# Performance work log

Hardware: AMD Instinct MI355X
Metric: run time of the kernel (lower is better)

The kernel has to match this reference:

```python
import jax, jax.numpy as jnp
import numpy as np

NC = 30      # n_centres in HyperNetwork RBFs
WIDTH = 64
D = 32
BATCH = 1048576


def _rbf_linear(t, centres, log_sigmas, lin_w, lin_b):
    # RBF_CNF(in_features=1) followed by nn.Linear; gaussian basis exp(-d^2)
    d = jnp.abs(t - centres[:, 0]) / jnp.exp(log_sigmas)   # (NC,) via broadcast of t (1,)
    phi = jnp.exp(-d * d)
    return phi @ lin_w.T + lin_b                            # (out_features,)


def setup_inputs() -> dict:
    key = jax.random.key(0)
    blocksize = WIDTH * D
    ks = jax.random.split(key, 10)

    def lin(k, out_f, in_f):
        bound = 1.0 / np.sqrt(in_f).astype(np.float32)
        kw, kb = jax.random.split(k)
        w = jax.random.uniform(kw, (out_f, in_f), jnp.float32, -bound, bound)
        b = jax.random.uniform(kb, (out_f,), jnp.float32, -bound, bound)
        return w, b

    W_lin_w, W_lin_b = lin(ks[0], blocksize, NC)
    U_lin_w, U_lin_b = lin(ks[1], blocksize, NC)
    B_lin_w, B_lin_b = lin(ks[2], WIDTH, NC)
    return dict(
        t=jax.random.uniform(ks[3], (1,), jnp.float32),
        z=jax.random.normal(ks[4], (BATCH, D), jnp.float32),
        logp_z=jnp.zeros((BATCH, 1), jnp.float32),
        W_centres=jax.random.normal(ks[5], (NC, 1), jnp.float32),
        W_log_sigmas=jnp.zeros((NC,), jnp.float32),
        W_lin_w=W_lin_w, W_lin_b=W_lin_b,
        U_centres=jax.random.normal(ks[6], (NC, 1), jnp.float32),
        U_log_sigmas=jnp.zeros((NC,), jnp.float32),
        U_lin_w=U_lin_w, U_lin_b=U_lin_b,
        B_centres=jax.random.normal(ks[7], (NC, 1), jnp.float32),
        B_log_sigmas=jnp.zeros((NC,), jnp.float32),
        B_lin_w=B_lin_w, B_lin_b=B_lin_b,
    )


def reference(t, z, logp_z,
              W_centres, W_log_sigmas, W_lin_w, W_lin_b,
              U_centres, U_log_sigmas, U_lin_w, U_lin_b,
              B_centres, B_log_sigmas, B_lin_w, B_lin_b):
    # Hypernetwork-generated weights at time t
    Wt = _rbf_linear(t, W_centres, W_log_sigmas, W_lin_w, W_lin_b).reshape(WIDTH, D)
    Ut = _rbf_linear(t, U_centres, U_log_sigmas, U_lin_w, U_lin_b).reshape(WIDTH, D)
    Bt = _rbf_linear(t, B_centres, B_log_sigmas, B_lin_w, B_lin_b)  # (WIDTH,)

    # h[w,b] = tanh(z_b . Wt_w + Bt_w); torch builds (WIDTH,B,D) copies, we fuse
    h = jnp.tanh(z @ Wt.T + Bt)        # (B, WIDTH)
    dz_dt = (h @ Ut) / WIDTH           # mean over width -> (B, D)

    # Exact Jacobian trace (what trace_df_dz computes via an autograd loop):
    # d dz_dt[b,i] / d z[b,i] = mean_w (1 - h[b,w]^2) * Wt[w,i] * Ut[w,i]
    wu = jnp.sum(Wt * Ut, axis=1)                 # (WIDTH,)
    trace = ((1.0 - h * h) @ wu) / WIDTH          # (B,)
    dlogp_z_dt = -trace[:, None]                  # (B, 1)
    return dz_dt, dlogp_z_dt
```

## Files before the change

### kernel.cpp

```cpp
#include <hip/hip_runtime.h>
#include <hip/hip_bf16.h>

#define NC 30
#define WIDTH 64
#define DD 32
#define BATCH_N 1048576

typedef __bf16 bf16x8 __attribute__((ext_vector_type(8)));
typedef __bf16 bf16x4 __attribute__((ext_vector_type(4)));
typedef float f32x4 __attribute__((ext_vector_type(4)));

__device__ __forceinline__ bf16x8 pack_bf8(float4 a, float4 b) {
    bf16x8 r;
    r[0] = (__bf16)a.x; r[1] = (__bf16)a.y; r[2] = (__bf16)a.z; r[3] = (__bf16)a.w;
    r[4] = (__bf16)b.x; r[5] = (__bf16)b.y; r[6] = (__bf16)b.z; r[7] = (__bf16)b.w;
    return r;
}

__global__ void hyper_rows(
    const float* __restrict__ t,
    const float* __restrict__ Wc, const float* __restrict__ Wls,
    const float* __restrict__ Ww, const float* __restrict__ Wb,
    const float* __restrict__ Uc, const float* __restrict__ Uls,
    const float* __restrict__ Uw, const float* __restrict__ Ub,
    const float* __restrict__ Bc, const float* __restrict__ Bls,
    const float* __restrict__ Bw, const float* __restrict__ Bb,
    float* __restrict__ outWt, float* __restrict__ outUtT,
    float* __restrict__ outBt, float* __restrict__ outwu)
{
    __shared__ float phiW[NC], phiU[NC], phiB[NC];
    const float tv = t[0];
    const int tid = threadIdx.x;
    if (tid < NC) {
        float dW = fabsf(tv - Wc[tid]) * __expf(-Wls[tid]);
        phiW[tid] = __expf(-dW * dW);
        float dU = fabsf(tv - Uc[tid]) * __expf(-Uls[tid]);
        phiU[tid] = __expf(-dU * dU);
        float dB = fabsf(tv - Bc[tid]) * __expf(-Bls[tid]);
        phiB[tid] = __expf(-dB * dB);
    }
    __syncthreads();
    const int j = blockIdx.x * blockDim.x + tid;
    float aw = Wb[j];
    float au = Ub[j];
    #pragma unroll
    for (int k = 0; k < NC; ++k) {
        aw += phiW[k] * Ww[j * NC + k];
        au += phiU[k] * Uw[j * NC + k];
    }
    outWt[j] = aw;
    const int w = j >> 5, i = j & 31;
    outUtT[i * WIDTH + w] = au * 0.015625f;

    float p = aw * au;
    #pragma unroll
    for (int off = 1; off < 32; off <<= 1) p += __shfl_xor(p, off, 64);
    if ((tid & 31) == 0) outwu[w] = p * 0.015625f;

    if (blockIdx.x == 0 && tid < WIDTH) {
        float ab = Bb[tid];
        #pragma unroll
        for (int k = 0; k < NC; ++k) ab += phiB[k] * Bw[tid * NC + k];
        outBt[tid] = ab;
    }
}

__global__ __launch_bounds__(256, 4) void cnf_main(
    const float* __restrict__ z,
    const float* __restrict__ Wt,
    const float* __restrict__ UtT,
    const float* __restrict__ Bt, const float* __restrict__ wu,
    float* __restrict__ dz, float* __restrict__ dlogp)
{
    __shared__ __bf16 hbuf[4][16][72];
    const int tid  = threadIdx.x;
    const int wave = tid >> 6;
    const int lane = tid & 63;
    const int l15  = lane & 15;
    const int quad = lane >> 4;
    __bf16 (*hl)[72] = hbuf[wave];

    bf16x8 bW[4];
    #pragma unroll
    for (int t4 = 0; t4 < 4; ++t4) {
        const float4* p = (const float4*)(Wt + (t4 * 16 + l15) * DD + quad * 8);
        bW[t4] = pack_bf8(p[0], p[1]);
    }
    bf16x8 bU[2][2];
    #pragma unroll
    for (int c = 0; c < 2; ++c)
        #pragma unroll
        for (int t2 = 0; t2 < 2; ++t2) {
            const float4* p = (const float4*)(UtT + (t2 * 16 + l15) * WIDTH + c * 32 + quad * 8);
            bU[c][t2] = pack_bf8(p[0], p[1]);
        }
    const float TWO_LOG2E = 2.8853900817779268f;
    float bt2[16], wu4[16];
    #pragma unroll
    for (int t4 = 0; t4 < 4; ++t4)
        #pragma unroll
        for (int r = 0; r < 4; ++r) {
            const int wdx = t4 * 16 + quad * 4 + r;
            bt2[t4 * 4 + r] = TWO_LOG2E * Bt[wdx];
            wu4[t4 * 4 + r] = 4.0f * wu[wdx];
        }

    const size_t gw = (size_t)blockIdx.x * 4 + wave;
    const float* zp = z + (gw * 128 + l15) * DD + quad * 8;

    float4 za = ((const float4*)zp)[0];
    float4 zb = ((const float4*)zp)[1];
    const f32x4 zero = {0.f, 0.f, 0.f, 0.f};

    for (int it = 0; it < 8; ++it) {
        float4 na = {0,0,0,0}, nb = {0,0,0,0};
        if (it < 7) {
            const float4* np = (const float4*)(zp + 16 * DD);
            na = np[0]; nb = np[1];
        }

        bf16x8 aZ = pack_bf8(za, zb);
        f32x4 accS[4];
        #pragma unroll
        for (int t4 = 0; t4 < 4; ++t4)
            accS[t4] = __builtin_amdgcn_mfma_f32_16x16x32_bf16(bW[t4], aZ, zero, 0, 0, 0);

        float part = 0.f;
        #pragma unroll
        for (int t4 = 0; t4 < 4; ++t4) {
            bf16x4 hp;
            #pragma unroll
            for (int r = 0; r < 4; ++r) {
                const float f = fmaf(accS[t4][r], TWO_LOG2E, bt2[t4 * 4 + r]);
                const float e = exp2f(f);
                const float u = __builtin_amdgcn_rcpf(e + 1.0f);
                const float h = fmaf(-2.0f, u, 1.0f);
                part = fmaf(fmaf(-u, u, u), wu4[t4 * 4 + r], part);
                hp[r] = (__bf16)h;
            }
            *(bf16x4*)(&hl[l15][t4 * 16 + quad * 4]) = hp;
        }

        bf16x8 aH0 = *(const bf16x8*)&hl[l15][quad * 8];
        bf16x8 aH1 = *(const bf16x8*)&hl[l15][32 + quad * 8];
        f32x4 accD[2];
        #pragma unroll
        for (int t2 = 0; t2 < 2; ++t2) {
            f32x4 c0 = __builtin_amdgcn_mfma_f32_16x16x32_bf16(aH0, bU[0][t2], zero, 0, 0, 0);
            accD[t2]  = __builtin_amdgcn_mfma_f32_16x16x32_bf16(aH1, bU[1][t2], c0, 0, 0, 0);
        }

        part += __shfl_xor(part, 16, 64);
        part += __shfl_xor(part, 32, 64);

        const size_t row0 = gw * 128 + (size_t)it * 16;
        if (quad == 0) dlogp[row0 + l15] = -part;

        #pragma unroll
        for (int t2 = 0; t2 < 2; ++t2)
            #pragma unroll
            for (int r = 0; r < 4; ++r)
                dz[(row0 + quad * 4 + r) * DD + t2 * 16 + l15] = accD[t2][r];

        za = na; zb = nb;
        zp += 16 * DD;
    }
}

extern "C" void kernel_launch(void* const* d_in, const int* in_sizes, int n_in,
                              void* d_out, int out_size, void* d_ws, size_t ws_size,
                              hipStream_t stream)
{
    const float* t   = (const float*)d_in[0];
    const float* z   = (const float*)d_in[1];
    const float* Wc  = (const float*)d_in[3];
    const float* Wls = (const float*)d_in[4];
    const float* Ww  = (const float*)d_in[5];
    const float* Wb  = (const float*)d_in[6];
    const float* Uc  = (const float*)d_in[7];
    const float* Uls = (const float*)d_in[8];
    const float* Uw  = (const float*)d_in[9];
    const float* Ub  = (const float*)d_in[10];
    const float* Bc  = (const float*)d_in[11];
    const float* Bls = (const float*)d_in[12];
    const float* Bw  = (const float*)d_in[13];
    const float* Bb  = (const float*)d_in[14];

    float* wsWt  = (float*)d_ws;
    float* wsUtT = wsWt + 2048;
    float* wsBt  = wsUtT + 2048;
    float* wswu  = wsBt + 64;

    hyper_rows<<<16, 128, 0, stream>>>(t, Wc, Wls, Ww, Wb, Uc, Uls, Uw, Ub,
                                       Bc, Bls, Bw, Bb, wsWt, wsUtT, wsBt, wswu);

    float* dz = (float*)d_out;
    float* dlogp = dz + (size_t)BATCH_N * DD;
    cnf_main<<<2048, 256, 0, stream>>>(z, wsWt, wsUtT, wsBt, wswu, dz, dlogp);
}
```

Baseline: 282.1 us.

## Replace LDS transpose of h with permlane swaps and vectorize dz stores

The activation tile h is no longer written to shared memory and read back in the MFMA A-operand layout. It is rearranged in registers with permlane32/permlane16 swaps, and the second MFMA takes its operands in swapped order so the output is transposed. That transpose lets each lane store dz as two float4 writes instead of eight scalar strided stores. The change removes LDS traffic and improves store coalescing, but it relies on the permlane builtins being available and on the lane mapping being correct.

```diff
diff --git a/kernel.cpp b/kernel.cpp
--- a/kernel.cpp
+++ b/kernel.cpp
@@ -9,6 +9,8 @@
 typedef __bf16 bf16x8 __attribute__((ext_vector_type(8)));
 typedef __bf16 bf16x4 __attribute__((ext_vector_type(4)));
 typedef float f32x4 __attribute__((ext_vector_type(4)));
+typedef unsigned int uint32x2 __attribute__((ext_vector_type(2)));
+typedef unsigned int uint32x4 __attribute__((ext_vector_type(4)));
 
 __device__ __forceinline__ bf16x8 pack_bf8(float4 a, float4 b) {
     bf16x8 r;
@@ -72,13 +74,11 @@
     const float* __restrict__ Bt, const float* __restrict__ wu,
     float* __restrict__ dz, float* __restrict__ dlogp)
 {
-    __shared__ __bf16 hbuf[4][16][72];
     const int tid  = threadIdx.x;
     const int wave = tid >> 6;
     const int lane = tid & 63;
     const int l15  = lane & 15;
     const int quad = lane >> 4;
-    __bf16 (*hl)[72] = hbuf[wave];
 
     bf16x8 bW[4];
     #pragma unroll
@@ -126,6 +126,7 @@
             accS[t4] = __builtin_amdgcn_mfma_f32_16x16x32_bf16(bW[t4], aZ, zero, 0, 0, 0);
 
         float part = 0.f;
+        unsigned P[4][2];
         #pragma unroll
         for (int t4 = 0; t4 < 4; ++t4) {
             bf16x4 hp;
@@ -138,16 +139,29 @@
                 part = fmaf(fmaf(-u, u, u), wu4[t4 * 4 + r], part);
                 hp[r] = (__bf16)h;
             }
-            *(bf16x4*)(&hl[l15][t4 * 16 + quad * 4]) = hp;
-        }
-
-        bf16x8 aH0 = *(const bf16x8*)&hl[l15][quad * 8];
-        bf16x8 aH1 = *(const bf16x8*)&hl[l15][32 + quad * 8];
+            uint32x2 pp = __builtin_bit_cast(uint32x2, hp);
+            P[t4][0] = pp[0]; P[t4][1] = pp[1];
+        }
+
+        auto w32a = __builtin_amdgcn_permlane32_swap(P[0][0], P[1][0], false, false);
+        auto w32b = __builtin_amdgcn_permlane32_swap(P[0][1], P[1][1], false, false);
+        auto w16a = __builtin_amdgcn_permlane16_swap(w32a[0], w32a[1], false, false);
+        auto w16b = __builtin_amdgcn_permlane16_swap(w32b[0], w32b[1], false, false);
+        uint32x4 u0 = {w16a[0], w16b[0], w16a[1], w16b[1]};
+        bf16x8 aH0 = __builtin_bit_cast(bf16x8, u0);
+
+        auto x32a = __builtin_amdgcn_permlane32_swap(P[2][0], P[3][0], false, false);
+        auto x32b = __builtin_amdgcn_permlane32_swap(P[2][1], P[3][1], false, false);
+        auto x16a = __builtin_amdgcn_permlane16_swap(x32a[0], x32a[1], false, false);
+        auto x16b = __builtin_amdgcn_permlane16_swap(x32b[0], x32b[1], false, false);
+        uint32x4 u1 = {x16a[0], x16b[0], x16a[1], x16b[1]};
+        bf16x8 aH1 = __builtin_bit_cast(bf16x8, u1);
+
         f32x4 accD[2];
         #pragma unroll
         for (int t2 = 0; t2 < 2; ++t2) {
-            f32x4 c0 = __builtin_amdgcn_mfma_f32_16x16x32_bf16(aH0, bU[0][t2], zero, 0, 0, 0);
-            accD[t2]  = __builtin_amdgcn_mfma_f32_16x16x32_bf16(aH1, bU[1][t2], c0, 0, 0, 0);
+            f32x4 cc = __builtin_amdgcn_mfma_f32_16x16x32_bf16(bU[0][t2], aH0, zero, 0, 0, 0);
+            accD[t2] = __builtin_amdgcn_mfma_f32_16x16x32_bf16(bU[1][t2], aH1, cc, 0, 0, 0);
         }
 
         part += __shfl_xor(part, 16, 64);
@@ -157,10 +171,11 @@
         if (quad == 0) dlogp[row0 + l15] = -part;
 
         #pragma unroll
-        for (int t2 = 0; t2 < 2; ++t2)
-            #pragma unroll
-            for (int r = 0; r < 4; ++r)
-                dz[(row0 + quad * 4 + r) * DD + t2 * 16 + l15] = accD[t2][r];
+        for (int t2 = 0; t2 < 2; ++t2) {
+            float4 v;
+            v.x = accD[t2][0]; v.y = accD[t2][1]; v.z = accD[t2][2]; v.w = accD[t2][3];
+            *(float4*)(dz + (row0 + l15) * DD + t2 * 16 + quad * 4) = v;
+        }
 
         za = na; zb = nb;
         zp += 16 * DD;
```

New measurement: 281.8 us. No clear change (-0.1%).
